# Kernel optimization log

Hardware: AMD Instinct MI355X
Metric: run time of the kernel (lower is better)

## Reference

```python
import jax, jax.numpy as jnp
import numpy as np

B, S, D, H, DH = 2, 2048, 1024, 16, 64


def setup_inputs() -> dict:
    key = jax.random.key(0)
    ks = jax.random.split(key, 8)
    std = 0.02
    Q = jax.random.normal(ks[0], (B, S, D), jnp.float32)
    K = jax.random.normal(ks[1], (B, S, D), jnp.float32)
    V = jax.random.normal(ks[2], (B, S, D), jnp.float32)
    # 0/1 float mask, 1 = masked out (causal upper triangle), shape [B, S, S]
    causal = jnp.triu(jnp.ones((S, S), jnp.float32), k=1)
    attn_mask = jnp.broadcast_to(causal, (B, S, S))
    Wq = jax.random.normal(ks[3], (D, H * DH), jnp.float32) * std
    Wk = jax.random.normal(ks[4], (D, H * DH), jnp.float32) * std
    Wv = jax.random.normal(ks[5], (D, H * DH), jnp.float32) * std
    Wo = jax.random.normal(ks[6], (H * DH, D), jnp.float32) * std
    bq = jnp.zeros((H * DH,), jnp.float32)
    bk = jnp.zeros((H * DH,), jnp.float32)
    bv = jnp.zeros((H * DH,), jnp.float32)
    bo = jnp.zeros((D,), jnp.float32)
    return dict(Q=Q, K=K, V=V, attn_mask=attn_mask,
                Wq=Wq, bq=bq, Wk=Wk, bk=bk, Wv=Wv, bv=bv, Wo=Wo, bo=bo)


def reference(Q, K, V, attn_mask, Wq, bq, Wk, bk, Wv, bv, Wo, bo):
    b = Q.shape[0]
    # projections + split heads: [B, S, H*DH] -> [B, H, S, DH]
    def heads(x, W, bias):
        y = x @ W + bias
        return y.reshape(b, -1, H, DH).transpose(0, 2, 1, 3)
    Qh = heads(Q, Wq, bq)
    Kh = heads(K, Wk, bk)
    Vh = heads(V, Wv, bv)
    scale = jnp.sqrt(jnp.asarray(DH, jnp.float32))
    # [B, H, Sq, Sk]
    scores = jnp.einsum('bhqd,bhkd->bhqk', Qh, Kh) / scale
    scores = scores - 1e9 * attn_mask[:, None, :, :]
    probs = jax.nn.softmax(scores, axis=-1)
    out = jnp.einsum('bhqk,bhkd->bhqd', probs, Vh)  # [B, H, Sq, DH]
    out = out.transpose(0, 2, 1, 3).reshape(b, -1, H * DH)
    return out @ Wo + bo
```

## Files before the change

kernel.cpp:

```cpp
#include <hip/hip_runtime.h>
#include <hip/hip_bf16.h>

#define S_LEN 2048
#define NH 16
#define DHD 64

typedef __attribute__((ext_vector_type(8))) short bf16x8;
typedef __attribute__((ext_vector_type(4))) float f32x4;

__device__ __forceinline__ f32x4 mfma16(bf16x8 a, bf16x8 b, f32x4 c) {
  return __builtin_amdgcn_mfma_f32_16x16x32_bf16(a, b, c, 0, 0, 0);
}

union Pack8 { int4 v; __hip_bfloat16 h[8]; };

__device__ __forceinline__ unsigned pack_bf16(float lo, float hi) {
  union { __hip_bfloat16 b; unsigned short s; } a0, a1;
  a0.b = __float2bfloat16(lo);
  a1.b = __float2bfloat16(hi);
  return (unsigned)a0.s | ((unsigned)a1.s << 16);
}

__device__ __forceinline__ void gload_lds16(const void* g, void* l) {
  __builtin_amdgcn_global_load_lds(
      (const __attribute__((address_space(1))) void*)(unsigned long long)g,
      (__attribute__((address_space(3))) void*)(unsigned long long)l,
      16, 0, 0);
}

__global__ __launch_bounds__(256) void cast3_bf16(
    const float* __restrict__ Qx, const float* __restrict__ Kx,
    const float* __restrict__ Vx, __hip_bfloat16* __restrict__ Xb) {
  const int z = blockIdx.y;
  const float* X = z == 0 ? Qx : z == 1 ? Kx : Vx;
  __hip_bfloat16* O = Xb + (size_t)z * 4194304u;
  const size_t base = ((size_t)blockIdx.x * 256 + threadIdx.x) * 8;
  const float4 f0 = *(const float4*)&X[base];
  const float4 f1 = *(const float4*)&X[base + 4];
  Pack8 p;
  p.h[0] = __float2bfloat16(f0.x); p.h[1] = __float2bfloat16(f0.y);
  p.h[2] = __float2bfloat16(f0.z); p.h[3] = __float2bfloat16(f0.w);
  p.h[4] = __float2bfloat16(f1.x); p.h[5] = __float2bfloat16(f1.y);
  p.h[6] = __float2bfloat16(f1.z); p.h[7] = __float2bfloat16(f1.w);
  *(int4*)&O[base] = p.v;
}

__global__ __launch_bounds__(256) void transpose_cast(
    const float* __restrict__ W0, const float* __restrict__ W1,
    const float* __restrict__ W2, const float* __restrict__ W3,
    __hip_bfloat16* __restrict__ T0, __hip_bfloat16* __restrict__ T1,
    __hip_bfloat16* __restrict__ T2, __hip_bfloat16* __restrict__ T3) {
  __shared__ float t[32][33];
  const float* W;
  __hip_bfloat16* T;
  switch (blockIdx.z) {
    case 0: W = W0; T = T0; break;
    case 1: W = W1; T = T1; break;
    case 2: W = W2; T = T2; break;
    default: W = W3; T = T3; break;
  }
  const int tx = threadIdx.x, ty = threadIdx.y;
  const int c = blockIdx.x * 32 + tx;
  const int r0 = blockIdx.y * 32;
#pragma unroll
  for (int i = ty; i < 32; i += 8) t[i][tx] = W[(r0 + i) * 1024 + c];
  __syncthreads();
  const int c0 = blockIdx.x * 32;
#pragma unroll
  for (int i = ty; i < 32; i += 8)
    T[(c0 + i) * 1024 + (r0 + tx)] = __float2bfloat16(t[tx][i]);
}

__global__ __launch_bounds__(256) void qkv_gemm(
    const __hip_bfloat16* __restrict__ Xb,
    const __hip_bfloat16* __restrict__ WqT, const __hip_bfloat16* __restrict__ WkT,
    const __hip_bfloat16* __restrict__ WvT,
    const float* __restrict__ bq, const float* __restrict__ bk,
    const float* __restrict__ bv,
    __hip_bfloat16* __restrict__ Qh, __hip_bfloat16* __restrict__ Kh,
    __hip_bfloat16* __restrict__ Vt) {
  __shared__ __hip_bfloat16 sA[128 * 64];
  __shared__ __hip_bfloat16 sB[128 * 64];
  const int K = 1024;
  const int yy = blockIdx.y;
  const int sel = yy >> 3;
  const int m0 = blockIdx.x * 128;
  const int n0 = (yy & 7) * 128;
  const __hip_bfloat16* A = Xb + (size_t)sel * 4194304u;
  const __hip_bfloat16* Bt = sel == 0 ? WqT : sel == 1 ? WkT : WvT;
  const float* bias = sel == 0 ? bq : sel == 1 ? bk : bv;
  __hip_bfloat16* outp = sel == 0 ? Qh : sel == 1 ? Kh : Vt;
  const float scale = sel == 0 ? 0.18033688011112042f : 1.0f;
  const int tid = threadIdx.x;
  const int lane = tid & 63;
  const int wv = tid >> 6;
  const int wm = (wv >> 1) * 64;
  const int wn = (wv & 1) * 64;
  const int rq = lane & 15;
  const int kg = lane >> 4;
  const int brow = lane >> 3;
  const int bcol = (lane & 7) * 8;
  f32x4 acc[4][4] = {};
  for (int k0 = 0; k0 < K; k0 += 64) {
#pragma unroll
    for (int i2 = 0; i2 < 4; ++i2) {
      const int ci = wv * 4 + i2;
      gload_lds16(A + (size_t)(m0 + ci * 8 + brow) * K + k0 + bcol,
                  (char*)sA + ci * 1024);
      gload_lds16(Bt + (size_t)(n0 + ci * 8 + brow) * K + k0 + bcol,
                  (char*)sB + ci * 1024);
    }
    __syncthreads();
#pragma unroll
    for (int kk = 0; kk < 2; ++kk) {
      bf16x8 af[4], bfr[4];
      const int kcol = kk * 32 + kg * 8;
#pragma unroll
      for (int mi = 0; mi < 4; ++mi)
        af[mi] = *(const bf16x8*)&sA[(wm + mi * 16 + rq) * 64 + kcol];
#pragma unroll
      for (int ni = 0; ni < 4; ++ni)
        bfr[ni] = *(const bf16x8*)&sB[(wn + ni * 16 + rq) * 64 + kcol];
#pragma unroll
      for (int mi = 0; mi < 4; ++mi)
#pragma unroll
        for (int ni = 0; ni < 4; ++ni)
          acc[mi][ni] = mfma16(af[mi], bfr[ni], acc[mi][ni]);
    }
    __syncthreads();
  }
  const int cr = (lane >> 4) << 2;
  const int cc = lane & 15;
#pragma unroll
  for (int ni = 0; ni < 4; ++ni) {
    const int col = n0 + wn + ni * 16 + cc;
    const float bv_ = bias[col];
#pragma unroll
    for (int mi = 0; mi < 4; ++mi) {
      const int rowb = m0 + wm + mi * 16 + cr;
#pragma unroll
      for (int r = 0; r < 4; ++r) {
        const int row = rowb + r;
        const float v = (acc[mi][ni][r] + bv_) * scale;
        const int b = row >> 11, s = row & 2047, h = col >> 6, dh = col & 63;
        const __hip_bfloat16 hv = __float2bfloat16(v);
        if (sel < 2)
          outp[((b * NH + h) * S_LEN + s) * DHD + dh] = hv;
        else
          outp[((b * NH + h) * DHD + dh) * S_LEN + s] = hv;
      }
    }
  }
}

#define LDP 72

__global__ __launch_bounds__(256) void out_gemm(
    const __hip_bfloat16* __restrict__ Aptr, const __hip_bfloat16* __restrict__ Bt,
    const float* __restrict__ bias, float* __restrict__ outp) {
  __shared__ __hip_bfloat16 sA[128 * LDP];
  __shared__ __hip_bfloat16 sB[128 * LDP];
  const int K = 1024;
  const int m0 = blockIdx.x * 128;
  const int n0 = blockIdx.y * 128;
  const int tid = threadIdx.x;
  const int lane = tid & 63;
  const int wv = tid >> 6;
  const int wm = (wv >> 1) * 64;
  const int wn = (wv & 1) * 64;
  const int rq = lane & 15;
  const int kg = lane >> 4;
  f32x4 acc[4][4] = {};
  for (int k0 = 0; k0 < K; k0 += 64) {
#pragma unroll
    for (int j = 0; j < 4; ++j) {
      const int cid = j * 256 + tid;
      const int row = cid >> 3;
      const int kc = (cid & 7) * 8;
      *(int4*)&sA[row * LDP + kc] = *(const int4*)(Aptr + (m0 + row) * K + k0 + kc);
      *(int4*)&sB[row * LDP + kc] = *(const int4*)(Bt + (n0 + row) * K + k0 + kc);
    }
    __syncthreads();
#pragma unroll
    for (int kk = 0; kk < 2; ++kk) {
      bf16x8 af[4], bfr[4];
      const int kcol = kk * 32 + kg * 8;
#pragma unroll
      for (int mi = 0; mi < 4; ++mi)
        af[mi] = *(const bf16x8*)&sA[(wm + mi * 16 + rq) * LDP + kcol];
#pragma unroll
      for (int ni = 0; ni < 4; ++ni)
        bfr[ni] = *(const bf16x8*)&sB[(wn + ni * 16 + rq) * LDP + kcol];
#pragma unroll
      for (int mi = 0; mi < 4; ++mi)
#pragma unroll
        for (int ni = 0; ni < 4; ++ni)
          acc[mi][ni] = mfma16(af[mi], bfr[ni], acc[mi][ni]);
    }
    __syncthreads();
  }
  const int cr = (lane >> 4) << 2;
  const int cc = lane & 15;
#pragma unroll
  for (int ni = 0; ni < 4; ++ni) {
    const int col = n0 + wn + ni * 16 + cc;
    const float bv = bias[col];
#pragma unroll
    for (int mi = 0; mi < 4; ++mi) {
      const int rowb = m0 + wm + mi * 16 + cr;
#pragma unroll
      for (int r = 0; r < 4; ++r)
        outp[(rowb + r) * 1024 + col] = acc[mi][ni][r] + bv;
    }
  }
}

#define SLOT 2304
#define NSLOT 320

__global__ __launch_bounds__(256) void attn_fwd(
    const __hip_bfloat16* __restrict__ Qh, const __hip_bfloat16* __restrict__ Kh,
    const __hip_bfloat16* __restrict__ Vt, __hip_bfloat16* __restrict__ AttO,
    unsigned char* __restrict__ Part) {
  __shared__ __hip_bfloat16 sK[64 * 72];
  __shared__ __hip_bfloat16 sV[64 * 72];
  const int tid = threadIdx.x;
  const int lane = tid & 63;
  const int wv = tid >> 6;
  const int h = blockIdx.y, b = blockIdx.z;
  const int bh = b * NH + h;
  const int u = 79 - (int)blockIdx.x;
  int j, s;
  if (u < 8)       { j = u; s = 0; }
  else if (u < 24) { int v = u - 8;  j = 8 + (v >> 1);  s = v & 1; }
  else if (u < 48) { int v = u - 24; int q3 = v / 3; j = 16 + q3; s = v - 3 * q3; }
  else             { int v = u - 48; j = 24 + (v >> 2); s = v & 3; }
  const int ns = (j >> 3) + 1;
  const int kv_beg = s * 512;
  const int kv_end = min(kv_beg + 512, j * 64 + 64);
  const int nt = (kv_end - kv_beg + 63) >> 6;

  const int i_tile = 4 * j + wv;
  const int q0 = i_tile * 16;
  const int qmax = q0 + 15;
  const __hip_bfloat16* Qb = Qh + bh * (S_LEN * DHD);
  const __hip_bfloat16* Kb = Kh + bh * (S_LEN * DHD);
  const __hip_bfloat16* Vb = Vt + bh * (DHD * S_LEN);
  const int c = lane & 15;
  const int g = lane >> 4;
  const bf16x8 qf0 = *(const bf16x8*)&Qb[(q0 + c) * DHD + g * 8];
  const bf16x8 qf1 = *(const bf16x8*)&Qb[(q0 + c) * DHD + 32 + g * 8];
  f32x4 o[4] = {};
  float m_run = -1e30f, l_run = 0.f;
  const int idx_lo = c + ((lane & 16) << 1);
  const int idx_hi = idx_lo + 16;
  const int lim0 = q0 + c - (g << 2);
  const bool hi_half = (lane & 32) != 0;

  const int srow = tid >> 2;
  const int scol = (tid & 3) << 4;
  int4 ka0, ka1, va0, va1;
#define ISSUE_LOADS(KV0)                                                  \
  ka0 = *(const int4*)&Kb[(KV0 + srow) * DHD + scol];                     \
  ka1 = *(const int4*)&Kb[(KV0 + srow) * DHD + scol + 8];                 \
  va0 = *(const int4*)&Vb[srow * S_LEN + (KV0) + scol];                   \
  va1 = *(const int4*)&Vb[srow * S_LEN + (KV0) + scol + 8];
#define STORE_LDS()                                                       \
  *(int4*)&sK[srow * 72 + scol] = ka0;                                    \
  *(int4*)&sK[srow * 72 + scol + 8] = ka1;                                \
  *(int4*)&sV[srow * 72 + scol] = va0;                                    \
  *(int4*)&sV[srow * 72 + scol + 8] = va1;

  ISSUE_LOADS(kv_beg);
  STORE_LDS();
  __syncthreads();

  for (int t = 0; t < nt; ++t) {
    const int kv0 = kv_beg + t * 64;
    const bool havenext = (t + 1 < nt);
    if (havenext) { ISSUE_LOADS(kv0 + 64); }
    if (kv0 <= qmax) {
      f32x4 sc[4] = {};
#pragma unroll
      for (int fi = 0; fi < 4; ++fi) {
        const bf16x8 ka = *(const bf16x8*)&sK[(fi * 16 + c) * 72 + g * 8];
        const bf16x8 kb = *(const bf16x8*)&sK[(fi * 16 + c) * 72 + 32 + g * 8];
        sc[fi] = mfma16(ka, qf0, sc[fi]);
        sc[fi] = mfma16(kb, qf1, sc[fi]);
      }
      if (kv0 + 63 > q0) {
        const int lim = lim0 - kv0;
#pragma unroll
        for (int fi = 0; fi < 4; ++fi)
#pragma unroll
          for (int r = 0; r < 4; ++r)
            if (fi * 16 + r > lim) sc[fi][r] = -1e30f;
      }
      float pm = fmaxf(fmaxf(fmaxf(sc[0][0], sc[0][1]), fmaxf(sc[0][2], sc[0][3])),
                       fmaxf(fmaxf(sc[1][0], sc[1][1]), fmaxf(sc[1][2], sc[1][3])));
      pm = fmaxf(pm, fmaxf(fmaxf(fmaxf(sc[2][0], sc[2][1]), fmaxf(sc[2][2], sc[2][3])),
                           fmaxf(fmaxf(sc[3][0], sc[3][1]), fmaxf(sc[3][2], sc[3][3]))));
      pm = fmaxf(pm, __shfl_xor(pm, 16));
      pm = fmaxf(pm, __shfl_xor(pm, 32));
      if (__any(pm > m_run + 8.0f)) {
        const float mn = fmaxf(m_run, pm);
        const float al = __builtin_amdgcn_exp2f(m_run - mn);
        m_run = mn;
        l_run *= al;
#pragma unroll
        for (int jj = 0; jj < 4; ++jj)
#pragma unroll
          for (int r = 0; r < 4; ++r) o[jj][r] *= al;
      }
      f32x4 p[4];
      float ps = 0.f;
#pragma unroll
      for (int fi = 0; fi < 4; ++fi) {
#pragma unroll
        for (int r = 0; r < 4; ++r) {
          p[fi][r] = __builtin_amdgcn_exp2f(sc[fi][r] - m_run);
          ps += p[fi][r];
        }
      }
      ps += __shfl_xor(ps, 16);
      ps += __shfl_xor(ps, 32);
      l_run += ps;
      unsigned w0[4], w1[4];
#pragma unroll
      for (int fi = 0; fi < 4; ++fi) {
        w0[fi] = pack_bf16(p[fi][0], p[fi][1]);
        w1[fi] = pack_bf16(p[fi][2], p[fi][3]);
      }
#pragma unroll
      for (int kk = 0; kk < 2; ++kk) {
        const int fA = 2 * kk, fB = 2 * kk + 1;
        union { unsigned w[4]; bf16x8 v; } pa;
        unsigned a0 = __shfl((int)w0[fA], idx_lo), b0 = __shfl((int)w0[fB], idx_lo);
        unsigned a1 = __shfl((int)w1[fA], idx_lo), b1 = __shfl((int)w1[fB], idx_lo);
        unsigned a2 = __shfl((int)w0[fA], idx_hi), b2 = __shfl((int)w0[fB], idx_hi);
        unsigned a3 = __shfl((int)w1[fA], idx_hi), b3 = __shfl((int)w1[fB], idx_hi);
        pa.w[0] = hi_half ? b0 : a0;
        pa.w[1] = hi_half ? b1 : a1;
        pa.w[2] = hi_half ? b2 : a2;
        pa.w[3] = hi_half ? b3 : a3;
#pragma unroll
        for (int jj = 0; jj < 4; ++jj) {
          const bf16x8 vf = *(const bf16x8*)&sV[(jj * 16 + c) * 72 + kk * 32 + g * 8];
          o[jj] = mfma16(vf, pa.v, o[jj]);
        }
      }
    }
    if (havenext) {
      __syncthreads();
      STORE_LDS();
      __syncthreads();
    }
  }

  if (ns == 1) {
    const float inv = 1.0f / l_run;
    __hip_bfloat16* op = AttO + (size_t)(b * S_LEN + q0 + c) * 1024 + h * DHD;
#pragma unroll
    for (int jj = 0; jj < 4; ++jj) {
      unsigned lo = pack_bf16(o[jj][0] * inv, o[jj][1] * inv);
      unsigned hi = pack_bf16(o[jj][2] * inv, o[jj][3] * inv);
      *(uint2*)&op[jj * 16 + (g << 2)] = make_uint2(lo, hi);
    }
  } else {
    int xr;
    if (i_tile < 64) xr = 32 + 2 * (i_tile - 32) + s;
    else if (i_tile < 96) xr = 96 + 3 * (i_tile - 64) + s;
    else xr = 192 + 4 * (i_tile - 96) + s;
    unsigned char* slot = Part + (size_t)(bh * NSLOT + xr) * SLOT;
    __hip_bfloat16* ob = (__hip_bfloat16*)slot;
#pragma unroll
    for (int jj = 0; jj < 4; ++jj) {
      unsigned lo = pack_bf16(o[jj][0], o[jj][1]);
      unsigned hi = pack_bf16(o[jj][2], o[jj][3]);
      *(uint2*)&ob[c * DHD + jj * 16 + (g << 2)] = make_uint2(lo, hi);
    }
    if (lane < 16) {
      *(float*)(slot + 2048 + lane * 4) = m_run;
      *(float*)(slot + 2112 + lane * 4) = l_run;
    }
  }
#undef ISSUE_LOADS
#undef STORE_LDS
}

__global__ __launch_bounds__(64) void attn_combine(
    const unsigned char* __restrict__ Part, __hip_bfloat16* __restrict__ AttO) {
  const int i = 32 + (int)blockIdx.x;
  const int h = blockIdx.y, b = blockIdx.z;
  const int bh = b * NH + h;
  const int ns = (i >> 5) + 1;
  int xr0;
  if (i < 64) xr0 = 32 + 2 * (i - 32);
  else if (i < 96) xr0 = 96 + 3 * (i - 64);
  else xr0 = 192 + 4 * (i - 96);
  const int lane = threadIdx.x;
  const int q = lane >> 2, qa = lane & 3;
  const unsigned char* base = Part + (size_t)(bh * NSLOT + xr0) * SLOT;
  float M = -1e30f;
  for (int s = 0; s < ns; ++s)
    M = fmaxf(M, *(const float*)(base + s * SLOT + 2048 + q * 4));
  float O[16] = {};
  float L = 0.f;
  for (int s = 0; s < ns; ++s) {
    const unsigned char* sp = base + s * SLOT;
    const float ms = *(const float*)(sp + 2048 + q * 4);
    const float ls = *(const float*)(sp + 2112 + q * 4);
    const float scale = __builtin_amdgcn_exp2f(ms - M);
    L += ls * scale;
    Pack8 w0, w1;
    w0.v = *(const int4*)(sp + (q * DHD + qa * 16) * 2);
    w1.v = *(const int4*)(sp + (q * DHD + qa * 16 + 8) * 2);
#pragma unroll
    for (int e = 0; e < 8; ++e) {
      O[e] += __bfloat162float(w0.h[e]) * scale;
      O[8 + e] += __bfloat162float(w1.h[e]) * scale;
    }
  }
  const float inv = 1.0f / L;
  Pack8 r0, r1;
#pragma unroll
  for (int e = 0; e < 8; ++e) {
    r0.h[e] = __float2bfloat16(O[e] * inv);
    r1.h[e] = __float2bfloat16(O[8 + e] * inv);
  }
  __hip_bfloat16* op = AttO + (size_t)(b * S_LEN + i * 16 + q) * 1024 + h * DHD + qa * 16;
  *(int4*)op = r0.v;
  *(int4*)(op + 8) = r1.v;
}

extern "C" void kernel_launch(void* const* d_in, const int* in_sizes, int n_in,
                              void* d_out, int out_size, void* d_ws, size_t ws_size,
                              hipStream_t stream) {
  const float* Qx = (const float*)d_in[0];
  const float* Kx = (const float*)d_in[1];
  const float* Vx = (const float*)d_in[2];
  const float* Wq = (const float*)d_in[4];
  const float* bq = (const float*)d_in[5];
  const float* Wk = (const float*)d_in[6];
  const float* bk = (const float*)d_in[7];
  const float* Wv = (const float*)d_in[8];
  const float* bv = (const float*)d_in[9];
  const float* Wo = (const float*)d_in[10];
  const float* bo = (const float*)d_in[11];

  __hip_bfloat16* ws = (__hip_bfloat16*)d_ws;
  __hip_bfloat16* WqT = ws;
  __hip_bfloat16* WkT = ws + (1u << 20);
  __hip_bfloat16* WvT = ws + (2u << 20);
  __hip_bfloat16* WoT = ws + (3u << 20);
  __hip_bfloat16* Qh  = ws + (4u << 20);
  __hip_bfloat16* Kh  = ws + (8u << 20);
  __hip_bfloat16* Vt  = ws + (12u << 20);
  __hip_bfloat16* AttO = ws + (16u << 20);
  unsigned char* Part = (unsigned char*)(ws + (20u << 20));
  __hip_bfloat16* Xb = (__hip_bfloat16*)(Part + (size_t)32 * NSLOT * SLOT);

  cast3_bf16<<<dim3(2048, 3), 256, 0, stream>>>(Qx, Kx, Vx, Xb);
  transpose_cast<<<dim3(32, 32, 4), dim3(32, 8), 0, stream>>>(
      Wq, Wk, Wv, Wo, WqT, WkT, WvT, WoT);
  qkv_gemm<<<dim3(32, 24), 256, 0, stream>>>(
      Xb, WqT, WkT, WvT, bq, bk, bv, Qh, Kh, Vt);
  attn_fwd<<<dim3(80, 16, 2), 256, 0, stream>>>(Qh, Kh, Vt, AttO, Part);
  attn_combine<<<dim3(96, 16, 2), 64, 0, stream>>>(Part, AttO);
  out_gemm<<<dim3(32, 8), 256, 0, stream>>>(AttO, WoT, bo, (float*)d_out);
}
```

Measured before the change: 161.6 us.

## Fuse fp32-to-bf16 input cast into QKV GEMM tile loads; use LDS-direct loads in out GEMM

Removes the separate cast kernel that wrote bf16 copies of Q, K and V. The QKV GEMM now reads fp32 activations directly, converts them in registers and stores them into a padded LDS tile. This drops one launch and a full write-and-reread of the bf16 intermediates. The cost is that each GEMM tile now reads fp32 data, and the 8 column-tile blocks sharing each row tile repeat the conversion. Separately, the output GEMM switches from register-staged copies to global_load_lds direct loads with unpadded tiles, which may bring back LDS bank conflicts.

```diff
diff --git a/kernel.cpp b/kernel.cpp
--- a/kernel.cpp
+++ b/kernel.cpp
@@ -26,23 +26,6 @@
       (const __attribute__((address_space(1))) void*)(unsigned long long)g,
       (__attribute__((address_space(3))) void*)(unsigned long long)l,
       16, 0, 0);
-}
-
-__global__ __launch_bounds__(256) void cast3_bf16(
-    const float* __restrict__ Qx, const float* __restrict__ Kx,
-    const float* __restrict__ Vx, __hip_bfloat16* __restrict__ Xb) {
-  const int z = blockIdx.y;
-  const float* X = z == 0 ? Qx : z == 1 ? Kx : Vx;
-  __hip_bfloat16* O = Xb + (size_t)z * 4194304u;
-  const size_t base = ((size_t)blockIdx.x * 256 + threadIdx.x) * 8;
-  const float4 f0 = *(const float4*)&X[base];
-  const float4 f1 = *(const float4*)&X[base + 4];
-  Pack8 p;
-  p.h[0] = __float2bfloat16(f0.x); p.h[1] = __float2bfloat16(f0.y);
-  p.h[2] = __float2bfloat16(f0.z); p.h[3] = __float2bfloat16(f0.w);
-  p.h[4] = __float2bfloat16(f1.x); p.h[5] = __float2bfloat16(f1.y);
-  p.h[6] = __float2bfloat16(f1.z); p.h[7] = __float2bfloat16(f1.w);
-  *(int4*)&O[base] = p.v;
 }
 
 __global__ __launch_bounds__(256) void transpose_cast(
@@ -71,22 +54,25 @@
     T[(c0 + i) * 1024 + (r0 + tx)] = __float2bfloat16(t[tx][i]);
 }
 
+#define LDP 72
+
 __global__ __launch_bounds__(256) void qkv_gemm(
-    const __hip_bfloat16* __restrict__ Xb,
+    const float* __restrict__ Qx, const float* __restrict__ Kx,
+    const float* __restrict__ Vx,
     const __hip_bfloat16* __restrict__ WqT, const __hip_bfloat16* __restrict__ WkT,
     const __hip_bfloat16* __restrict__ WvT,
     const float* __restrict__ bq, const float* __restrict__ bk,
     const float* __restrict__ bv,
     __hip_bfloat16* __restrict__ Qh, __hip_bfloat16* __restrict__ Kh,
     __hip_bfloat16* __restrict__ Vt) {
-  __shared__ __hip_bfloat16 sA[128 * 64];
+  __shared__ __hip_bfloat16 sA[128 * LDP];
   __shared__ __hip_bfloat16 sB[128 * 64];
   const int K = 1024;
   const int yy = blockIdx.y;
   const int sel = yy >> 3;
   const int m0 = blockIdx.x * 128;
   const int n0 = (yy & 7) * 128;
-  const __hip_bfloat16* A = Xb + (size_t)sel * 4194304u;
+  const float* X = sel == 0 ? Qx : sel == 1 ? Kx : Vx;
   const __hip_bfloat16* Bt = sel == 0 ? WqT : sel == 1 ? WkT : WvT;
   const float* bias = sel == 0 ? bq : sel == 1 ? bk : bv;
   __hip_bfloat16* outp = sel == 0 ? Qh : sel == 1 ? Kh : Vt;
@@ -105,10 +91,23 @@
 #pragma unroll
     for (int i2 = 0; i2 < 4; ++i2) {
       const int ci = wv * 4 + i2;
-      gload_lds16(A + (size_t)(m0 + ci * 8 + brow) * K + k0 + bcol,
-                  (char*)sA + ci * 1024);
       gload_lds16(Bt + (size_t)(n0 + ci * 8 + brow) * K + k0 + bcol,
                   (char*)sB + ci * 1024);
+    }
+#pragma unroll
+    for (int j = 0; j < 4; ++j) {
+      const int cid = j * 256 + tid;
+      const int row = cid >> 3;
+      const int kc = (cid & 7) * 8;
+      const float* ap = X + (size_t)(m0 + row) * K + k0 + kc;
+      float4 f0 = *(const float4*)ap;
+      float4 f1 = *(const float4*)(ap + 4);
+      Pack8 p;
+      p.h[0] = __float2bfloat16(f0.x); p.h[1] = __float2bfloat16(f0.y);
+      p.h[2] = __float2bfloat16(f0.z); p.h[3] = __float2bfloat16(f0.w);
+      p.h[4] = __float2bfloat16(f1.x); p.h[5] = __float2bfloat16(f1.y);
+      p.h[6] = __float2bfloat16(f1.z); p.h[7] = __float2bfloat16(f1.w);
+      *(int4*)&sA[row * LDP + kc] = p.v;
     }
     __syncthreads();
 #pragma unroll
@@ -117,7 +116,7 @@
       const int kcol = kk * 32 + kg * 8;
 #pragma unroll
       for (int mi = 0; mi < 4; ++mi)
-        af[mi] = *(const bf16x8*)&sA[(wm + mi * 16 + rq) * 64 + kcol];
+        af[mi] = *(const bf16x8*)&sA[(wm + mi * 16 + rq) * LDP + kcol];
 #pragma unroll
       for (int ni = 0; ni < 4; ++ni)
         bfr[ni] = *(const bf16x8*)&sB[(wn + ni * 16 + rq) * 64 + kcol];
@@ -153,13 +152,11 @@
   }
 }
 
-#define LDP 72
-
 __global__ __launch_bounds__(256) void out_gemm(
     const __hip_bfloat16* __restrict__ Aptr, const __hip_bfloat16* __restrict__ Bt,
     const float* __restrict__ bias, float* __restrict__ outp) {
-  __shared__ __hip_bfloat16 sA[128 * LDP];
-  __shared__ __hip_bfloat16 sB[128 * LDP];
+  __shared__ __hip_bfloat16 sA[128 * 64];
+  __shared__ __hip_bfloat16 sB[128 * 64];
   const int K = 1024;
   const int m0 = blockIdx.x * 128;
   const int n0 = blockIdx.y * 128;
@@ -170,15 +167,17 @@
   const int wn = (wv & 1) * 64;
   const int rq = lane & 15;
   const int kg = lane >> 4;
+  const int brow = lane >> 3;
+  const int bcol = (lane & 7) * 8;
   f32x4 acc[4][4] = {};
   for (int k0 = 0; k0 < K; k0 += 64) {
 #pragma unroll
-    for (int j = 0; j < 4; ++j) {
-      const int cid = j * 256 + tid;
-      const int row = cid >> 3;
-      const int kc = (cid & 7) * 8;
-      *(int4*)&sA[row * LDP + kc] = *(const int4*)(Aptr + (m0 + row) * K + k0 + kc);
-      *(int4*)&sB[row * LDP + kc] = *(const int4*)(Bt + (n0 + row) * K + k0 + kc);
+    for (int i2 = 0; i2 < 4; ++i2) {
+      const int ci = wv * 4 + i2;
+      gload_lds16(Aptr + (size_t)(m0 + ci * 8 + brow) * K + k0 + bcol,
+                  (char*)sA + ci * 1024);
+      gload_lds16(Bt + (size_t)(n0 + ci * 8 + brow) * K + k0 + bcol,
+                  (char*)sB + ci * 1024);
     }
     __syncthreads();
 #pragma unroll
@@ -187,10 +186,10 @@
       const int kcol = kk * 32 + kg * 8;
 #pragma unroll
       for (int mi = 0; mi < 4; ++mi)
-        af[mi] = *(const bf16x8*)&sA[(wm + mi * 16 + rq) * LDP + kcol];
+        af[mi] = *(const bf16x8*)&sA[(wm + mi * 16 + rq) * 64 + kcol];
 #pragma unroll
       for (int ni = 0; ni < 4; ++ni)
-        bfr[ni] = *(const bf16x8*)&sB[(wn + ni * 16 + rq) * LDP + kcol];
+        bfr[ni] = *(const bf16x8*)&sB[(wn + ni * 16 + rq) * 64 + kcol];
 #pragma unroll
       for (int mi = 0; mi < 4; ++mi)
 #pragma unroll
@@ -458,13 +457,11 @@
   __hip_bfloat16* Vt  = ws + (12u << 20);
   __hip_bfloat16* AttO = ws + (16u << 20);
   unsigned char* Part = (unsigned char*)(ws + (20u << 20));
-  __hip_bfloat16* Xb = (__hip_bfloat16*)(Part + (size_t)32 * NSLOT * SLOT);
-
-  cast3_bf16<<<dim3(2048, 3), 256, 0, stream>>>(Qx, Kx, Vx, Xb);
+
   transpose_cast<<<dim3(32, 32, 4), dim3(32, 8), 0, stream>>>(
       Wq, Wk, Wv, Wo, WqT, WkT, WvT, WoT);
   qkv_gemm<<<dim3(32, 24), 256, 0, stream>>>(
-      Xb, WqT, WkT, WvT, bq, bk, bv, Qh, Kh, Vt);
+      Qx, Kx, Vx, WqT, WkT, WvT, bq, bk, bv, Qh, Kh, Vt);
   attn_fwd<<<dim3(80, 16, 2), 256, 0, stream>>>(Qh, Kh, Vt, AttO, Part);
   attn_combine<<<dim3(96, 16, 2), 64, 0, stream>>>(Part, AttO);
   out_gemm<<<dim3(32, 8), 256, 0, stream>>>(AttO, WoT, bo, (float*)d_out);
```

After: 154.8 us. 1.04x faster.
